# Kernel optimization log

Measured on AMD Instinct MI355X. Metric: run time of the kernel, lower is better.

The kernel has to match this reference:

```python
import jax, jax.numpy as jnp
import numpy as np

# Product-key memory config (matches init_kwargs)
HEADS = 4
K_DIM = 512          # per-head query/key dim; split in two halves of 256
HALF = K_DIM // 2
V_DIM = 512
SUBSIZE = 512        # sub-keys per bank; value table size = SUBSIZE**2
SIZE = SUBSIZE * SUBSIZE
TOPK = 8
TEMP = 1.0
B, T = 4, 2048


def setup_inputs() -> dict:
    key = jax.random.key(0)
    kq, kk, kv = jax.random.split(key, 3)
    bound = 1.0 / np.sqrt(K_DIM)  # reset_parameters: uniform(-1/sqrt(k_dim), 1/sqrt(k_dim))
    query = jax.random.normal(kq, (B, T, HEADS * K_DIM), dtype=jnp.float32)
    keys = jax.random.uniform(kk, (2 * HEADS * SUBSIZE, HALF), dtype=jnp.float32,
                              minval=-bound, maxval=bound)
    # reset_parameters: normal(0, v_dim**-0.5)
    values = jax.random.normal(kv, (SIZE, V_DIM), dtype=jnp.float32) * (V_DIM ** -0.5)
    return {"query": query, "keys": keys, "values": values}


def reference(query, keys, values):
    """retrieve_values: product-key two-stage topk + softmax-weighted embedding bag.
    query: [B, T, HEADS*K_DIM]; keys: [2*HEADS*SUBSIZE, HALF]; values: [SIZE, V_DIM]
    returns retrieved values [B*T, V_DIM].
    """
    Bq, Tq = query.shape[:2]
    N = Bq * Tq
    q = query.reshape(N, HEADS, K_DIM)
    q1, q2 = q[..., :HALF], q[..., HALF:]
    k = keys.reshape(2, HEADS, SUBSIZE, HALF)

    # Sub-key score matmuls (the two 'cdist-like' searches)
    s1 = jnp.einsum('nhd,hsd->nhs', q1, k[0])       # [N, H, SUBSIZE]
    s2 = jnp.einsum('nhd,hsd->nhs', q2, k[1])       # [N, H, SUBSIZE]

    ts1, ti1 = jax.lax.top_k(s1, TOPK)               # [N, H, TOPK]
    ts2, ti2 = jax.lax.top_k(s2, TOPK)

    # Cartesian combination of the two topk sets, then global topk
    comb = (ts1[..., :, None] + ts2[..., None, :]).reshape(N, HEADS, TOPK * TOPK)
    scores, flat_idx = jax.lax.top_k(comb, TOPK)     # [N, H, TOPK]
    sel1 = jnp.take_along_axis(ti1, flat_idx // TOPK, axis=-1)
    sel2 = jnp.take_along_axis(ti2, flat_idx % TOPK, axis=-1)
    indices = sel1 * SUBSIZE + sel2                  # global value-table indices [N, H, TOPK]

    # score_transform: softmax over heads*topk (score_nonlinear='softmax')
    w = jax.nn.softmax(scores.reshape(N, HEADS * TOPK) / TEMP, axis=-1)

    # xformers_embedding_bag: weighted gather-sum over the huge value table
    gathered = values[indices.reshape(N, HEADS * TOPK)]   # [N, H*TOPK, V_DIM]
    vals = jnp.einsum('nk,nkd->nd', w, gathered)          # [N, V_DIM]
    return vals
```

## Files before the change

kernel.cpp:

```cpp
#include <hip/hip_runtime.h>
#include <hip/hip_bf16.h>
#include <math.h>

typedef unsigned short u16;
typedef __attribute__((ext_vector_type(8))) short short8;
typedef __attribute__((ext_vector_type(4))) float f32x4;

#define N_TOK   8192
#define N_HEADS 4
#define KDIM    512
#define HALFD   256
#define VDIM    512
#define SUBK    512
#define NCAND   16

__device__ __forceinline__ u16 f2bf(float f) {
    unsigned u = __float_as_uint(f);
    u += 0x7fffu + ((u >> 16) & 1u);
    return (u16)(u >> 16);
}

__global__ void k_convert(const float* __restrict__ in, u16* __restrict__ out, int n4) {
    int i = blockIdx.x * blockDim.x + threadIdx.x;
    int stride = gridDim.x * blockDim.x;
    for (; i < n4; i += stride) {
        float4 v = ((const float4*)in)[i];
        unsigned a = (unsigned)f2bf(v.x) | ((unsigned)f2bf(v.y) << 16);
        unsigned b = (unsigned)f2bf(v.z) | ((unsigned)f2bf(v.w) << 16);
        ((uint2*)out)[i] = make_uint2(a, b);
    }
}

__global__ __launch_bounds__(256) void k_score_topk(
    const u16* __restrict__ qb,
    const u16* __restrict__ kb,
    int* __restrict__ cand)
{
    __shared__ float sc[16 * 513];
    const int nb = blockIdx.x, h = blockIdx.y, half = blockIdx.z;
    const int tid = threadIdx.x;
    const int wave = tid >> 6, l = tid & 63;
    const int lr = l & 15, lk = l >> 4;

    const u16* qbase = qb + (size_t)(nb * 16 + lr) * (N_HEADS * KDIM) + h * KDIM + half * HALFD + lk * 8;
    short8 a[8];
#pragma unroll
    for (int kf = 0; kf < 8; ++kf)
        a[kf] = *(const short8*)(qbase + kf * 32);

    const u16* kbase = kb + (size_t)(half * N_HEADS + h) * SUBK * HALFD;
    for (int t = 0; t < 8; ++t) {
        int st = wave * 8 + t;
        const u16* kp = kbase + (size_t)(st * 16 + lr) * HALFD + lk * 8;
        short8 b[8];
#pragma unroll
        for (int kf = 0; kf < 8; ++kf)
            b[kf] = *(const short8*)(kp + kf * 32);
        f32x4 acc = {0.f, 0.f, 0.f, 0.f};
#pragma unroll
        for (int kf = 0; kf < 8; ++kf)
            acc = __builtin_amdgcn_mfma_f32_16x16x32_bf16(a[kf], b[kf], acc, 0, 0, 0);
#pragma unroll
        for (int r = 0; r < 4; ++r)
            sc[(lk * 4 + r) * 513 + st * 16 + lr] = acc[r];
    }
    __syncthreads();

    const int row = tid >> 4, sub = tid & 15;
    float tv[NCAND]; int ti[NCAND];
#pragma unroll
    for (int j = 0; j < NCAND; ++j) { tv[j] = -3e38f; ti[j] = 0; }
    for (int t = 0; t < 32; ++t) {
        int s = sub + (t << 4);
        float v = sc[row * 513 + s];
        if (v > tv[NCAND - 1]) {
#pragma unroll
            for (int j = NCAND - 1; j >= 0; --j) {
                bool cj = v > tv[j];
                bool cm = (j > 0) ? (v > tv[j - 1]) : false;
                float pv = (j > 0) ? tv[j - 1] : 0.f;
                int   pi = (j > 0) ? ti[j - 1] : 0;
                float nv = cj ? (cm ? pv : v) : tv[j];
                int   ni = cj ? (cm ? pi : s) : ti[j];
                tv[j] = nv; ti[j] = ni;
            }
        }
    }

    int keepidx = 0;
    for (int r = 0; r < NCAND; ++r) {
        float m = tv[0]; int mi = ti[0]; int ml = sub;
#pragma unroll
        for (int d = 1; d < 16; d <<= 1) {
            float ov = __shfl_xor(m, d, 16);
            int   oi = __shfl_xor(mi, d, 16);
            int   ol = __shfl_xor(ml, d, 16);
            if (ov > m || (ov == m && ol < ml)) { m = ov; mi = oi; ml = ol; }
        }
        if (sub == r) keepidx = mi;
        if (ml == sub) {
#pragma unroll
            for (int j = 0; j < NCAND - 1; ++j) { tv[j] = tv[j + 1]; ti[j] = ti[j + 1]; }
            tv[NCAND - 1] = -3e38f;
        }
    }
    int n = nb * 16 + row;
    cand[((size_t)n * 8 + (h * 2 + half)) * NCAND + sub] = keepidx;
}

__global__ __launch_bounds__(256) void k_refine(
    const float* __restrict__ query,
    const float* __restrict__ keys,
    const float* __restrict__ values,
    const int* __restrict__ cand,
    float* __restrict__ out)
{
    __shared__ double rv[8][16];
    __shared__ int    ri[8][16];
    __shared__ double tsv[8][8];
    __shared__ int    tsi[8][8];
    __shared__ double s_comb[32];
    __shared__ int    gidx[32];
    __shared__ float  wsm[32];

    const int n = blockIdx.x;
    const int tid = threadIdx.x;

    if (tid < 128) {
        int g = tid >> 4, j = tid & 15;
        int h = g >> 1, half = g & 1;
        int sidx = cand[((size_t)n * 8 + g) * NCAND + j];
        const float* qrow = query + (size_t)n * (N_HEADS * KDIM) + h * KDIM + half * HALFD;
        const float* krow = keys + ((size_t)(half * N_HEADS + h) * SUBK + sidx) * HALFD;
        double a0 = 0, a1 = 0, a2 = 0, a3 = 0;
        for (int d = 0; d < HALFD; d += 4) {
            float4 qv = *(const float4*)(qrow + d);
            float4 kv = *(const float4*)(krow + d);
            a0 = fma((double)qv.x, (double)kv.x, a0);
            a1 = fma((double)qv.y, (double)kv.y, a1);
            a2 = fma((double)qv.z, (double)kv.z, a2);
            a3 = fma((double)qv.w, (double)kv.w, a3);
        }
        rv[g][j] = (a0 + a1) + (a2 + a3);
        ri[g][j] = sidx;
    }
    __syncthreads();

    if (tid < 8) {
        int g = tid;
        unsigned used = 0;
        for (int r = 0; r < 8; ++r) {
            double best = -1e300; int bi = 0;
            for (int j = 0; j < 16; ++j) {
                double v = rv[g][j];
                if (!((used >> j) & 1u) && v > best) { best = v; bi = j; }
            }
            used |= 1u << bi;
            tsv[g][r] = best; tsi[g][r] = ri[g][bi];
        }
    }
    __syncthreads();

    if (tid < 4) {
        int h = tid;
        unsigned long long used = 0;
        for (int r = 0; r < 8; ++r) {
            double best = -1e300; int bf = 0;
            for (int f = 0; f < 64; ++f) {
                double c = tsv[h * 2][f >> 3] + tsv[h * 2 + 1][f & 7];
                if (!((used >> f) & 1ull) && c > best) { best = c; bf = f; }
            }
            used |= 1ull << bf;
            s_comb[h * 8 + r] = best;
            gidx[h * 8 + r] = tsi[h * 2][bf >> 3] * SUBK + tsi[h * 2 + 1][bf & 7];
        }
    }
    __syncthreads();

    if (tid == 0) {
        double m = -1e300;
        for (int k = 0; k < 32; ++k) m = fmax(m, s_comb[k]);
        double sum = 0;
        for (int k = 0; k < 32; ++k) { double e = exp(s_comb[k] - m); wsm[k] = (float)e; sum += e; }
        float inv = (float)(1.0 / sum);
        for (int k = 0; k < 32; ++k) wsm[k] *= inv;
    }
    __syncthreads();

    float acc0 = 0.f, acc1 = 0.f;
#pragma unroll 4
    for (int k = 0; k < 32; ++k) {
        const float* vr = values + (size_t)gidx[k] * VDIM;
        float w = wsm[k];
        acc0 = fmaf(w, vr[tid], acc0);
        acc1 = fmaf(w, vr[tid + 256], acc1);
    }
    out[(size_t)n * VDIM + tid] = acc0;
    out[(size_t)n * VDIM + 256 + tid] = acc1;
}

extern "C" void kernel_launch(void* const* d_in, const int* in_sizes, int n_in,
                              void* d_out, int out_size, void* d_ws, size_t ws_size,
                              hipStream_t stream) {
    const float* query  = (const float*)d_in[0];
    const float* keys   = (const float*)d_in[1];
    const float* values = (const float*)d_in[2];
    float* out = (float*)d_out;

    char* ws = (char*)d_ws;
    u16* qb   = (u16*)ws;
    u16* kb   = (u16*)(ws + 33554432);
    int* cand = (int*)(ws + 33554432 + 2097152);

    k_convert<<<4096, 256, 0, stream>>>(query, qb, (N_TOK * N_HEADS * KDIM) / 4);
    k_convert<<<512, 256, 0, stream>>>(keys, kb, (2 * N_HEADS * SUBK * HALFD) / 4);

    dim3 gB(N_TOK / 16, N_HEADS, 2);
    k_score_topk<<<gB, 256, 0, stream>>>(qb, kb, cand);

    k_refine<<<N_TOK, 256, 0, stream>>>(query, keys, values, cand, out);
}
```

Before: 469.1 us.

## Split refine into parallel select and batched gather kernels

The refine kernel's serial single-thread top-k, cartesian top-k and softmax become wave-parallel shuffle reductions, and the fp64 rescoring dot products are split across two lanes so all 256 threads work. The weighted value gather moves into its own kernel that issues sixteen float2 row loads at once to raise memory-level parallelism. This removes long serial phases where most of the block sat idle. The cost is an extra launch plus a round trip of indices and weights through global memory, and the softmax exponent is now computed in fp32 instead of fp64.

Measured after the change: 427.3 us. -8.9%, faster.

```diff
diff --git a/kernel.cpp b/kernel.cpp
--- a/kernel.cpp
+++ b/kernel.cpp
@@ -108,32 +108,33 @@
     cand[((size_t)n * 8 + (h * 2 + half)) * NCAND + sub] = keepidx;
 }
 
-__global__ __launch_bounds__(256) void k_refine(
+__global__ __launch_bounds__(256) void k_select(
     const float* __restrict__ query,
     const float* __restrict__ keys,
-    const float* __restrict__ values,
     const int* __restrict__ cand,
-    float* __restrict__ out)
+    int* __restrict__ gout,
+    float* __restrict__ wout)
 {
     __shared__ double rv[8][16];
     __shared__ int    ri[8][16];
     __shared__ double tsv[8][8];
     __shared__ int    tsi[8][8];
     __shared__ double s_comb[32];
-    __shared__ int    gidx[32];
-    __shared__ float  wsm[32];
+    __shared__ int    sgi[32];
 
     const int n = blockIdx.x;
     const int tid = threadIdx.x;
 
-    if (tid < 128) {
-        int g = tid >> 4, j = tid & 15;
-        int h = g >> 1, half = g & 1;
-        int sidx = cand[((size_t)n * 8 + g) * NCAND + j];
-        const float* qrow = query + (size_t)n * (N_HEADS * KDIM) + h * KDIM + half * HALFD;
-        const float* krow = keys + ((size_t)(half * N_HEADS + h) * SUBK + sidx) * HALFD;
+    {
+        const int dot = tid >> 1, part = tid & 1;
+        const int g = dot >> 4, j = dot & 15;
+        const int h = g >> 1, half = g & 1;
+        const int sidx = cand[((size_t)n * 8 + g) * NCAND + j];
+        const float* qrow = query + (size_t)n * (N_HEADS * KDIM) + h * KDIM + half * HALFD + part * 128;
+        const float* krow = keys + ((size_t)(half * N_HEADS + h) * SUBK + sidx) * HALFD + part * 128;
         double a0 = 0, a1 = 0, a2 = 0, a3 = 0;
-        for (int d = 0; d < HALFD; d += 4) {
+#pragma unroll 8
+        for (int d = 0; d < 128; d += 4) {
             float4 qv = *(const float4*)(qrow + d);
             float4 kv = *(const float4*)(krow + d);
             a0 = fma((double)qv.x, (double)kv.x, a0);
@@ -141,62 +142,97 @@
             a2 = fma((double)qv.z, (double)kv.z, a2);
             a3 = fma((double)qv.w, (double)kv.w, a3);
         }
-        rv[g][j] = (a0 + a1) + (a2 + a3);
-        ri[g][j] = sidx;
-    }
-    __syncthreads();
-
-    if (tid < 8) {
-        int g = tid;
-        unsigned used = 0;
+        double s = (a0 + a1) + (a2 + a3);
+        double o = __shfl_xor(s, 1);
+        if (part == 0) { rv[g][j] = s + o; ri[g][j] = sidx; }
+    }
+    __syncthreads();
+
+    if (tid < 128) {
+        const int g = tid >> 4, j = tid & 15;
+        double v = rv[g][j];
+        const int idx = ri[g][j];
         for (int r = 0; r < 8; ++r) {
-            double best = -1e300; int bi = 0;
-            for (int j = 0; j < 16; ++j) {
-                double v = rv[g][j];
-                if (!((used >> j) & 1u) && v > best) { best = v; bi = j; }
-            }
-            used |= 1u << bi;
-            tsv[g][r] = best; tsi[g][r] = ri[g][bi];
-        }
-    }
-    __syncthreads();
-
-    if (tid < 4) {
-        int h = tid;
-        unsigned long long used = 0;
+            double bv = v; int bj = j;
+#pragma unroll
+            for (int d = 1; d < 16; d <<= 1) {
+                double ov = __shfl_xor(bv, d, 16);
+                int    oj = __shfl_xor(bj, d, 16);
+                if (ov > bv || (ov == bv && oj < bj)) { bv = ov; bj = oj; }
+            }
+            int widx = __shfl(idx, bj, 16);
+            if (j == r) { tsv[g][r] = bv; tsi[g][r] = widx; }
+            if (j == bj) v = -1e300;
+        }
+    }
+    __syncthreads();
+
+    {
+        const int h = tid >> 6, f = tid & 63;
+        double c = tsv[h * 2][f >> 3] + tsv[h * 2 + 1][f & 7];
         for (int r = 0; r < 8; ++r) {
-            double best = -1e300; int bf = 0;
-            for (int f = 0; f < 64; ++f) {
-                double c = tsv[h * 2][f >> 3] + tsv[h * 2 + 1][f & 7];
-                if (!((used >> f) & 1ull) && c > best) { best = c; bf = f; }
-            }
-            used |= 1ull << bf;
-            s_comb[h * 8 + r] = best;
-            gidx[h * 8 + r] = tsi[h * 2][bf >> 3] * SUBK + tsi[h * 2 + 1][bf & 7];
-        }
-    }
-    __syncthreads();
-
-    if (tid == 0) {
-        double m = -1e300;
-        for (int k = 0; k < 32; ++k) m = fmax(m, s_comb[k]);
-        double sum = 0;
-        for (int k = 0; k < 32; ++k) { double e = exp(s_comb[k] - m); wsm[k] = (float)e; sum += e; }
-        float inv = (float)(1.0 / sum);
-        for (int k = 0; k < 32; ++k) wsm[k] *= inv;
-    }
-    __syncthreads();
-
-    float acc0 = 0.f, acc1 = 0.f;
-#pragma unroll 4
-    for (int k = 0; k < 32; ++k) {
-        const float* vr = values + (size_t)gidx[k] * VDIM;
-        float w = wsm[k];
-        acc0 = fmaf(w, vr[tid], acc0);
-        acc1 = fmaf(w, vr[tid + 256], acc1);
-    }
-    out[(size_t)n * VDIM + tid] = acc0;
-    out[(size_t)n * VDIM + 256 + tid] = acc1;
+            double bv = c; int bf = f;
+#pragma unroll
+            for (int d = 1; d < 64; d <<= 1) {
+                double ov = __shfl_xor(bv, d, 64);
+                int    of = __shfl_xor(bf, d, 64);
+                if (ov > bv || (ov == bv && of < bf)) { bv = ov; bf = of; }
+            }
+            if (f == r) {
+                s_comb[h * 8 + r] = bv;
+                sgi[h * 8 + r] = tsi[h * 2][bf >> 3] * SUBK + tsi[h * 2 + 1][bf & 7];
+            }
+            if (f == bf) c = -1e300;
+        }
+    }
+    __syncthreads();
+
+    if (tid < 32) {
+        const int k = tid;
+        double s = s_comb[k];
+        double m = s;
+#pragma unroll
+        for (int d = 1; d < 32; d <<= 1) m = fmax(m, __shfl_xor(m, d, 32));
+        float e = expf((float)(s - m));
+        float sum = e;
+#pragma unroll
+        for (int d = 1; d < 32; d <<= 1) sum += __shfl_xor(sum, d, 32);
+        wout[(size_t)n * 32 + k] = e / sum;
+        gout[(size_t)n * 32 + k] = sgi[k];
+    }
+}
+
+__global__ __launch_bounds__(256) void k_gather(
+    const float* __restrict__ values,
+    const int* __restrict__ gidx,
+    const float* __restrict__ w,
+    float* __restrict__ out)
+{
+    __shared__ float  ws_[32];
+    __shared__ size_t off_[32];
+    const int n = blockIdx.x;
+    const int tid = threadIdx.x;
+    if (tid < 32) {
+        ws_[tid] = w[(size_t)n * 32 + tid];
+        off_[tid] = (size_t)gidx[(size_t)n * 32 + tid] * VDIM;
+    }
+    __syncthreads();
+
+    float a0 = 0.f, a1 = 0.f;
+#pragma unroll
+    for (int kb = 0; kb < 32; kb += 16) {
+        float2 v[16];
+#pragma unroll
+        for (int k = 0; k < 16; ++k)
+            v[k] = ((const float2*)(values + off_[kb + k]))[tid];
+#pragma unroll
+        for (int k = 0; k < 16; ++k) {
+            float wk = ws_[kb + k];
+            a0 = fmaf(wk, v[k].x, a0);
+            a1 = fmaf(wk, v[k].y, a1);
+        }
+    }
+    ((float2*)(out + (size_t)n * VDIM))[tid] = make_float2(a0, a1);
 }
 
 extern "C" void kernel_launch(void* const* d_in, const int* in_sizes, int n_in,
@@ -208,9 +244,11 @@
     float* out = (float*)d_out;
 
     char* ws = (char*)d_ws;
-    u16* qb   = (u16*)ws;
-    u16* kb   = (u16*)(ws + 33554432);
-    int* cand = (int*)(ws + 33554432 + 2097152);
+    u16* qb    = (u16*)ws;
+    u16* kb    = (u16*)(ws + 33554432);
+    int* cand  = (int*)(ws + 33554432 + 2097152);
+    int* gidxb = (int*)(ws + 33554432 + 2097152 + 4194304);
+    float* wb  = (float*)(ws + 33554432 + 2097152 + 4194304 + 1048576);
 
     k_convert<<<4096, 256, 0, stream>>>(query, qb, (N_TOK * N_HEADS * KDIM) / 4);
     k_convert<<<512, 256, 0, stream>>>(keys, kb, (2 * N_HEADS * SUBK * HALFD) / 4);
@@ -218,5 +256,6 @@
     dim3 gB(N_TOK / 16, N_HEADS, 2);
     k_score_topk<<<gB, 256, 0, stream>>>(qb, kb, cand);
 
-    k_refine<<<N_TOK, 256, 0, stream>>>(query, keys, values, cand, out);
-}
+    k_select<<<N_TOK, 256, 0, stream>>>(query, keys, cand, gidxb, wb);
+    k_gather<<<N_TOK, 256, 0, stream>>>(values, gidxb, wb, out);
+}
```
